# Kernel tuning notes

Hardware: AMD Instinct MI355X
Metric: run time of the kernel (lower is better)

The kernel has to match this reference:

```python
import jax, jax.numpy as jnp
import numpy as np

N = 100000      # nodes
E = 400000      # edges per relation
R = 4           # relations
DIN = 128       # input feat dim
DH = 128        # hidden_feat
NC = 16         # n_classes


def setup_inputs() -> dict:
    key = jax.random.key(0)
    ks = jax.random.split(key, 9)
    s = lambda d: 1.0 / np.sqrt(d)
    return {
        "x":  jax.random.normal(ks[0], (N, DIN), jnp.float32),
        "W0": jax.random.normal(ks[1], (R, DIN, DH), jnp.float32) * s(DIN),
        "b0": jnp.zeros((R, DH), jnp.float32),
        "W1": jax.random.normal(ks[2], (R, DH, DH), jnp.float32) * s(DH),
        "b1": jnp.zeros((R, DH), jnp.float32),
        "W2": jax.random.normal(ks[3], (R, DH, NC), jnp.float32) * s(DH),
        "b2": jnp.zeros((R, NC), jnp.float32),
        "src": jax.random.randint(ks[4], (R, E), 0, N, jnp.int32),
        "dst": jax.random.randint(ks[5], (R, E), 0, N, jnp.int32),
    }


def _graph_conv(h, W, b, s, d, act):
    """DGL GraphConv, norm='both': deg_out^-1/2 gather-matmul-scatter deg_in^-1/2."""
    ones = jnp.ones(s.shape[0], h.dtype)
    deg_out = jnp.clip(jax.ops.segment_sum(ones, s, num_segments=N), 1.0)  # [N]
    deg_in  = jnp.clip(jax.ops.segment_sum(ones, d, num_segments=N), 1.0)  # [N]
    hn = (h * jax.lax.rsqrt(deg_out)[:, None]) @ W           # [N, dout] (mm before aggregate)
    agg = jax.ops.segment_sum(hn[s], d, num_segments=N)      # scatter-sum over edges
    out = agg * jax.lax.rsqrt(deg_in)[:, None] + b
    return jax.nn.relu(out) if act else out


def _hetero_layer(h, W, b, src, dst, act):
    # HeteroGraphConv(aggregate='mean'): per-relation GraphConv then mean over relations
    outs = [_graph_conv(h, W[r], b[r], src[r], dst[r], act) for r in range(R)]
    return sum(outs) / R


def reference(x, W0, b0, W1, b1, W2, b2, src, dst):
    h = _hetero_layer(x, W0, b0, src, dst, act=True)
    h = _hetero_layer(h, W1, b1, src, dst, act=True)
    return _hetero_layer(h, W2, b2, src, dst, act=False)  # [N, NC] logits for target_node type
```

## Files before the change

kernel.cpp:

```cpp
#include <hip/hip_runtime.h>


#define NNODES 100000
#define NEDGE  400000
#define NREL   4
#define DHID   128
#define NCLS   16
#define SCANB  98

typedef _Float16 f16x8 __attribute__((ext_vector_type(8)));
typedef _Float16 f16x4 __attribute__((ext_vector_type(4)));
typedef float    f32x4 __attribute__((ext_vector_type(4)));

__global__ void edge_hist(const int* __restrict__ src, const int* __restrict__ dst,
                          int* __restrict__ cnt_out, int* __restrict__ cnt_in) {
    int e = blockIdx.x * 256 + threadIdx.x;
    int r = blockIdx.y;
    if (e < NEDGE) {
        atomicAdd(&cnt_out[r * NNODES + src[r * NEDGE + e]], 1);
        atomicAdd(&cnt_in [r * NNODES + dst[r * NEDGE + e]], 1);
    }
}

__global__ void rs_fin(const int* __restrict__ cnt_out, const int* __restrict__ cnt_in,
                       float* __restrict__ rs_out, float* __restrict__ rs_in) {
    int i = blockIdx.x * 256 + threadIdx.x;
    if (i < NREL * NNODES) {
        rs_out[i] = rsqrtf(fmaxf((float)cnt_out[i], 1.0f));
        rs_in [i] = rsqrtf(fmaxf((float)cnt_in [i], 1.0f));
    }
}

__global__ void scan1(const int* __restrict__ cnt, int* __restrict__ part) {
    __shared__ int sh[256];
    int r = blockIdx.y, b = blockIdx.x, tid = threadIdx.x;
    int n0 = b * 1024 + tid * 4;
    int s = 0;
#pragma unroll
    for (int j = 0; j < 4; ++j) {
        int n = n0 + j;
        s += (n < NNODES) ? cnt[r * NNODES + n] : 0;
    }
    sh[tid] = s; __syncthreads();
    for (int off = 128; off > 0; off >>= 1) {
        if (tid < off) sh[tid] += sh[tid + off];
        __syncthreads();
    }
    if (tid == 0) part[r * SCANB + b] = sh[0];
}

__global__ void scan2(int* __restrict__ part) {
    __shared__ int sh[128];
    int r = blockIdx.x, tid = threadIdx.x;
    int v = (tid < SCANB) ? part[r * SCANB + tid] : 0;
    sh[tid] = v; __syncthreads();
    for (int off = 1; off < 128; off <<= 1) {
        int t = (tid >= off) ? sh[tid - off] : 0;
        __syncthreads();
        sh[tid] += t;
        __syncthreads();
    }
    if (tid < SCANB) part[r * SCANB + tid] = sh[tid] - v;
}

__global__ void scan3(const int* __restrict__ cnt, const int* __restrict__ part,
                      int* __restrict__ ofs) {
    __shared__ int sh[256];
    int r = blockIdx.y, b = blockIdx.x, tid = threadIdx.x;
    int n0 = b * 1024 + tid * 4;
    int v[4];
    int tsum = 0;
#pragma unroll
    for (int j = 0; j < 4; ++j) {
        int n = n0 + j;
        v[j] = (n < NNODES) ? cnt[r * NNODES + n] : 0;
        tsum += v[j];
    }
    sh[tid] = tsum; __syncthreads();
    for (int off = 1; off < 256; off <<= 1) {
        int t = (tid >= off) ? sh[tid - off] : 0;
        __syncthreads();
        sh[tid] += t;
        __syncthreads();
    }
    int base = part[r * SCANB + b] + sh[tid] - tsum;
#pragma unroll
    for (int j = 0; j < 4; ++j) {
        int n = n0 + j;
        if (n < NNODES) ofs[r * (NNODES + 1) + n] = base;
        base += v[j];
    }
    if (b == 0 && tid == 0) ofs[r * (NNODES + 1) + NNODES] = NEDGE;
}

__global__ void csr_fill(const int* __restrict__ src, const int* __restrict__ dst,
                         const int* __restrict__ ofs, int* __restrict__ cnt_in,
                         const float* __restrict__ rs_out, int2* __restrict__ csrw) {
    int e = blockIdx.x * 256 + threadIdx.x;
    int r = blockIdx.y;
    if (e < NEDGE) {
        int s = src[r * NEDGE + e], d = dst[r * NEDGE + e];
        int k = atomicSub(&cnt_in[r * NNODES + d], 1) - 1;
        int2 ew;
        ew.x = s;
        ew.y = __float_as_int(rs_out[r * NNODES + s]);
        csrw[(size_t)r * NEDGE + ofs[r * (NNODES + 1) + d] + k] = ew;
    }
}

__global__ void wsplit(const float* __restrict__ W, _Float16* __restrict__ whi,
                       _Float16* __restrict__ wlo) {
    int idx = blockIdx.x * 256 + threadIdx.x;
    int c = idx & 127, k = (idx >> 7) & 127, r = idx >> 14;
    float w = W[(size_t)r * 16384 + k * 128 + c];
    _Float16 hi = (_Float16)w;
    size_t o = (((size_t)r * 16 + (k >> 3)) * 128 + c) * 8 + (k & 7);
    whi[o] = hi;
    wlo[o] = (_Float16)(w - (float)hi);
}

__global__ void wsplit2(const float* __restrict__ W2, _Float16* __restrict__ wh,
                        _Float16* __restrict__ wl) {
    int idx = blockIdx.x * 256 + threadIdx.x;
    if (idx < NREL * DHID * NCLS) {
        int c = idx & 15, k = (idx >> 4) & 127, r = idx >> 11;
        float w = W2[idx];
        _Float16 hi = (_Float16)w;
        size_t o = ((size_t)(k >> 3) * 64 + r * 16 + c) * 8 + (k & 7);
        wh[o] = hi;
        wl[o] = (_Float16)(w - (float)hi);
    }
}

__global__ void xcvt(const float* __restrict__ x, _Float16* __restrict__ xh) {
    int i = blockIdx.x * 256 + threadIdx.x;
    if (i < NNODES * DHID / 4) {
        float4 v = ((const float4*)x)[i];
        f16x4 h = {(_Float16)v.x, (_Float16)v.y, (_Float16)v.z, (_Float16)v.w};
        *(f16x4*)&xh[(size_t)i * 4] = h;
    }
}

__global__ __launch_bounds__(512) void gconv(
        const _Float16* __restrict__ Hh, const float* __restrict__ rs_in,
        const int* __restrict__ ofs, const int2* __restrict__ csrw,
        const _Float16* __restrict__ Wt_hi, const _Float16* __restrict__ Wt_lo,
        const float* __restrict__ bias, _Float16* __restrict__ outH) {
    __shared__ _Float16 lhi[4 * 16 * 67 * 8];
    __shared__ int lofs[NREL][65];
    int tid = threadIdx.x;
    int lane = tid & 63, wid = tid >> 6;
    int wm = wid >> 2, wn = wid & 3;
    int r15 = lane & 15;
    int row0 = blockIdx.x * 64;

    if (tid < 4 * 65) {
        int rel = tid / 65, i = tid - rel * 65;
        int n = row0 + i;
        lofs[rel][i] = (n <= NNODES) ? ofs[rel * (NNODES + 1) + n] : NEDGE;
    }
    __syncthreads();

    {
        int lane16 = tid & 15;
        int grp    = tid >> 4;
        const _Float16* hb = Hh + (size_t)lane16 * 8;
        for (int idx = grp; idx < 256; idx += 32) {
            int rel = idx >> 6, rr = idx & 63;
            int row = row0 + rr;
            float acc[8] = {};
            if (row < NNODES) {
                int i = lofs[rel][rr], end = lofs[rel][rr + 1];
                const int2* cw = csrw + (size_t)rel * NEDGE;
                for (; i + 4 <= end; i += 4) {
                    int2 e0 = cw[i], e1 = cw[i + 1], e2 = cw[i + 2], e3 = cw[i + 3];
                    f16x8 v0 = *(const f16x8*)(hb + (size_t)e0.x * DHID);
                    f16x8 v1 = *(const f16x8*)(hb + (size_t)e1.x * DHID);
                    f16x8 v2 = *(const f16x8*)(hb + (size_t)e2.x * DHID);
                    f16x8 v3 = *(const f16x8*)(hb + (size_t)e3.x * DHID);
                    float w0 = __int_as_float(e0.y), w1 = __int_as_float(e1.y);
                    float w2 = __int_as_float(e2.y), w3 = __int_as_float(e3.y);
#pragma unroll
                    for (int j = 0; j < 8; ++j)
                        acc[j] += ((float)v0[j] * w0 + (float)v1[j] * w1)
                                + ((float)v2[j] * w2 + (float)v3[j] * w3);
                }
                for (; i < end; ++i) {
                    int2 e = cw[i];
                    f16x8 v = *(const f16x8*)(hb + (size_t)e.x * DHID);
                    float w = __int_as_float(e.y);
#pragma unroll
                    for (int j = 0; j < 8; ++j) acc[j] += (float)v[j] * w;
                }
                float rv = rs_in[rel * NNODES + row];
#pragma unroll
                for (int j = 0; j < 8; ++j) acc[j] *= rv;
            }
            f16x8 o;
#pragma unroll
            for (int j = 0; j < 8; ++j) o[j] = (_Float16)acc[j];
            *(f16x8*)&lhi[(((rel * 16 + lane16) * 67) + rr) * 8] = o;
        }
    }
    __syncthreads();

    f32x4 oacc[2][2] = {};
    int kb = lane >> 4;
    int rbase = wm * 32 + r15;
    int c = wn * 32 + r15;
    for (int rel = 0; rel < NREL; ++rel) {
        f32x4 acc4[2][2] = {};
#pragma unroll
        for (int kt = 0; kt < 4; ++kt) {
            const _Float16* bh = Wt_hi + ((size_t)rel * 16 + kt * 4 + kb) * 128 * 8;
            const _Float16* bl = Wt_lo + ((size_t)rel * 16 + kt * 4 + kb) * 128 * 8;
            f16x8 wh[2], wl[2], ah[2];
#pragma unroll
            for (int nf = 0; nf < 2; ++nf) {
                wh[nf] = *(const f16x8*)(bh + (size_t)(c + nf * 16) * 8);
                wl[nf] = *(const f16x8*)(bl + (size_t)(c + nf * 16) * 8);
            }
#pragma unroll
            for (int mf = 0; mf < 2; ++mf) {
                int li = (((rel * 16 + kt * 4 + kb) * 67) + rbase + mf * 16) * 8;
                ah[mf] = *(const f16x8*)&lhi[li];
            }
#pragma unroll
            for (int nf = 0; nf < 2; ++nf)
#pragma unroll
                for (int mf = 0; mf < 2; ++mf) {
                    acc4[mf][nf] = __builtin_amdgcn_mfma_f32_16x16x32_f16(ah[mf], wh[nf], acc4[mf][nf], 0, 0, 0);
                    acc4[mf][nf] = __builtin_amdgcn_mfma_f32_16x16x32_f16(ah[mf], wl[nf], acc4[mf][nf], 0, 0, 0);
                }
        }
        const float* b = bias + rel * DHID;
#pragma unroll
        for (int mf = 0; mf < 2; ++mf)
#pragma unroll
            for (int nf = 0; nf < 2; ++nf) {
                float bb = b[wn * 32 + nf * 16 + r15];
#pragma unroll
                for (int i = 0; i < 4; ++i)
                    oacc[mf][nf][i] += fmaxf(acc4[mf][nf][i] + bb, 0.f);
            }
    }

    int rsub = (lane >> 4) * 4;
#pragma unroll
    for (int mf = 0; mf < 2; ++mf)
#pragma unroll
        for (int i = 0; i < 4; ++i) {
            int row = row0 + wm * 32 + mf * 16 + rsub + i;
            if (row < NNODES) {
#pragma unroll
                for (int nf = 0; nf < 2; ++nf) {
                    int cc = wn * 32 + nf * 16 + r15;
                    outH[(size_t)row * DHID + cc] = (_Float16)(oacc[mf][nf][i] * 0.25f);
                }
            }
        }
}

__global__ __launch_bounds__(256) void gemm64h(const _Float16* __restrict__ Hh,
                                               const _Float16* __restrict__ W2h,
                                               const _Float16* __restrict__ W2l,
                                               float* __restrict__ hw) {
    int tid = threadIdx.x, lane = tid & 63, wid = tid >> 6;
    int row0 = blockIdx.x * 64;
    int arow = row0 + wid * 16 + (lane & 15);
    int kb = lane >> 4;
    f32x4 acc[4] = {};
#pragma unroll
    for (int kt = 0; kt < 4; ++kt) {
        f16x8 a = {};
        if (arow < NNODES)
            a = *(const f16x8*)&Hh[(size_t)arow * DHID + kt * 32 + kb * 8];
        const _Float16* bh = W2h + ((size_t)(kt * 4 + kb) * 64) * 8;
        const _Float16* bl = W2l + ((size_t)(kt * 4 + kb) * 64) * 8;
#pragma unroll
        for (int nf = 0; nf < 4; ++nf) {
            f16x8 wh = *(const f16x8*)(bh + (size_t)(nf * 16 + (lane & 15)) * 8);
            f16x8 wl = *(const f16x8*)(bl + (size_t)(nf * 16 + (lane & 15)) * 8);
            acc[nf] = __builtin_amdgcn_mfma_f32_16x16x32_f16(a, wh, acc[nf], 0, 0, 0);
            acc[nf] = __builtin_amdgcn_mfma_f32_16x16x32_f16(a, wl, acc[nf], 0, 0, 0);
        }
    }
    int rsub = (lane >> 4) * 4;
#pragma unroll
    for (int nf = 0; nf < 4; ++nf)
#pragma unroll
        for (int i = 0; i < 4; ++i) {
            int row = row0 + wid * 16 + rsub + i;
            if (row < NNODES) hw[(size_t)row * 64 + nf * 16 + (lane & 15)] = acc[nf][i];
        }
}

__global__ __launch_bounds__(256) void l2_out(const float* __restrict__ hw,
                                              const int* __restrict__ ofs,
                                              const int2* __restrict__ csrw,
                                              const float* __restrict__ rs_in,
                                              const float* __restrict__ b2,
                                              float* __restrict__ out) {
    int t = threadIdx.x;
    int d = blockIdx.x * 4 + (t >> 6);
    int lane = t & 63;
    int r = lane >> 4;
    int c = lane & 15;
    if (d >= NNODES) return;
    int i   = ofs[r * (NNODES + 1) + d];
    int end = ofs[r * (NNODES + 1) + d + 1];
    const int2* cw = csrw + (size_t)r * NEDGE;
    float acc = 0.f;
    for (; i + 2 <= end; i += 2) {
        int2 e0 = cw[i], e1 = cw[i + 1];
        acc += hw[(size_t)e0.x * 64 + r * NCLS + c] * __int_as_float(e0.y)
             + hw[(size_t)e1.x * 64 + r * NCLS + c] * __int_as_float(e1.y);
    }
    for (; i < end; ++i) {
        int2 e = cw[i];
        acc += hw[(size_t)e.x * 64 + r * NCLS + c] * __int_as_float(e.y);
    }
    float tot = acc * rs_in[r * NNODES + d] + b2[r * NCLS + c];
    tot += __shfl_xor(tot, 16, 64);
    tot += __shfl_xor(tot, 32, 64);
    if (r == 0) out[(size_t)d * NCLS + c] = tot * 0.25f;
}

extern "C" void kernel_launch(void* const* d_in, const int* in_sizes, int n_in,
                              void* d_out, int out_size, void* d_ws, size_t ws_size,
                              hipStream_t stream) {
    const float* x  = (const float*)d_in[0];
    const float* W0 = (const float*)d_in[1];
    const float* b0 = (const float*)d_in[2];
    const float* W1 = (const float*)d_in[3];
    const float* b1 = (const float*)d_in[4];
    const float* W2 = (const float*)d_in[5];
    const float* b2 = (const float*)d_in[6];
    const int*   src = (const int*)d_in[7];
    const int*   dst = (const int*)d_in[8];
    float* out = (float*)d_out;

    char* p = (char*)d_ws;
    int2* csrw   = (int2*)p;           p += sizeof(int2) * (size_t)NREL * NEDGE;
    float* hw    = (float*)p;          p += sizeof(float) * (size_t)NNODES * 64;
    int* cnt_out = (int*)p;            p += sizeof(int) * NREL * NNODES;
    int* cnt_in  = (int*)p;            p += sizeof(int) * NREL * NNODES;
    int* ofs     = (int*)p;            p += sizeof(int) * NREL * (NNODES + 1) + 12;
    int* part    = (int*)p;            p += sizeof(int) * NREL * 128;
    float* rs_out = (float*)p;         p += sizeof(float) * NREL * NNODES;
    float* rs_in  = (float*)p;         p += sizeof(float) * NREL * NNODES;
    _Float16* Wt0h = (_Float16*)p;     p += sizeof(_Float16) * NREL * DHID * DHID;
    _Float16* Wt0l = (_Float16*)p;     p += sizeof(_Float16) * NREL * DHID * DHID;
    _Float16* Wt1h = (_Float16*)p;     p += sizeof(_Float16) * NREL * DHID * DHID;
    _Float16* Wt1l = (_Float16*)p;     p += sizeof(_Float16) * NREL * DHID * DHID;
    _Float16* W2h  = (_Float16*)p;     p += sizeof(_Float16) * 16 * 64 * 8;
    _Float16* W2l  = (_Float16*)p;     p += sizeof(_Float16) * 16 * 64 * 8;
    _Float16* xh   = (_Float16*)p;     p += sizeof(_Float16) * (size_t)NNODES * DHID;
    _Float16* h1   = (_Float16*)p;     p += sizeof(_Float16) * (size_t)NNODES * DHID;
    _Float16* h2   = (_Float16*)p;     p += sizeof(_Float16) * (size_t)NNODES * DHID;

    hipMemsetAsync(cnt_out, 0, 2ull * NREL * NNODES * sizeof(int), stream);
    dim3 eg((NEDGE + 255) / 256, NREL);
    edge_hist<<<eg, 256, 0, stream>>>(src, dst, cnt_out, cnt_in);
    rs_fin<<<(NREL * NNODES + 255) / 256, 256, 0, stream>>>(cnt_out, cnt_in, rs_out, rs_in);
    dim3 sg(SCANB, NREL);
    scan1<<<sg, 256, 0, stream>>>(cnt_in, part);
    scan2<<<NREL, 128, 0, stream>>>(part);
    scan3<<<sg, 256, 0, stream>>>(cnt_in, part, ofs);
    csr_fill<<<eg, 256, 0, stream>>>(src, dst, ofs, cnt_in, rs_out, csrw);

    wsplit<<<256, 256, 0, stream>>>(W0, Wt0h, Wt0l);
    wsplit<<<256, 256, 0, stream>>>(W1, Wt1h, Wt1l);
    wsplit2<<<32, 256, 0, stream>>>(W2, W2h, W2l);
    xcvt<<<(NNODES * DHID / 4 + 255) / 256, 256, 0, stream>>>(x, xh);

    int gb = (NNODES + 63) / 64;

    gconv<<<gb, 512, 0, stream>>>(xh, rs_in, ofs, csrw, Wt0h, Wt0l, b0, h1);
    gconv<<<gb, 512, 0, stream>>>(h1, rs_in, ofs, csrw, Wt1h, Wt1l, b1, h2);

    gemm64h<<<gb, 256, 0, stream>>>(h2, W2h, W2l, hw);
    l2_out<<<(NNODES + 3) / 4, 256, 0, stream>>>(hw, ofs, csrw, rs_in, b2, out);
}
```

Baseline: 686.9 us.

## Interleave four rows per thread in gather, store layer-2 projection in fp16

```diff
diff --git a/kernel.cpp b/kernel.cpp
--- a/kernel.cpp
+++ b/kernel.cpp
@@ -165,13 +165,47 @@
         int lane16 = tid & 15;
         int grp    = tid >> 4;
         const _Float16* hb = Hh + (size_t)lane16 * 8;
-        for (int idx = grp; idx < 256; idx += 32) {
-            int rel = idx >> 6, rr = idx & 63;
-            int row = row0 + rr;
-            float acc[8] = {};
-            if (row < NNODES) {
-                int i = lofs[rel][rr], end = lofs[rel][rr + 1];
-                const int2* cw = csrw + (size_t)rel * NEDGE;
+#pragma unroll
+        for (int s = 0; s < 2; ++s) {
+            int rel[4], rr[4], ii[4], ee[4];
+            float acc[4][8] = {};
+#pragma unroll
+            for (int k = 0; k < 4; ++k) {
+                int u = grp + s * 128 + k * 32;
+                rel[k] = u >> 6; rr[k] = u & 63;
+                ii[k] = lofs[rel[k]][rr[k]];
+                ee[k] = lofs[rel[k]][rr[k] + 1];
+                if (row0 + rr[k] >= NNODES) { ii[k] = 0; ee[k] = 0; }
+            }
+            while (ii[0] + 2 <= ee[0] && ii[1] + 2 <= ee[1] &&
+                   ii[2] + 2 <= ee[2] && ii[3] + 2 <= ee[3]) {
+                int2 ed[4][2];
+                f16x8 v[4][2];
+#pragma unroll
+                for (int k = 0; k < 4; ++k) {
+                    const int2* cw = csrw + (size_t)rel[k] * NEDGE;
+                    ed[k][0] = cw[ii[k]];
+                    ed[k][1] = cw[ii[k] + 1];
+                }
+#pragma unroll
+                for (int k = 0; k < 4; ++k) {
+                    v[k][0] = *(const f16x8*)(hb + (size_t)ed[k][0].x * DHID);
+                    v[k][1] = *(const f16x8*)(hb + (size_t)ed[k][1].x * DHID);
+                }
+#pragma unroll
+                for (int k = 0; k < 4; ++k) {
+                    float w0 = __int_as_float(ed[k][0].y);
+                    float w1 = __int_as_float(ed[k][1].y);
+#pragma unroll
+                    for (int j = 0; j < 8; ++j)
+                        acc[k][j] += (float)v[k][0][j] * w0 + (float)v[k][1][j] * w1;
+                    ii[k] += 2;
+                }
+            }
+#pragma unroll
+            for (int k = 0; k < 4; ++k) {
+                const int2* cw = csrw + (size_t)rel[k] * NEDGE;
+                int i = ii[k], end = ee[k];
                 for (; i + 4 <= end; i += 4) {
                     int2 e0 = cw[i], e1 = cw[i + 1], e2 = cw[i + 2], e3 = cw[i + 3];
                     f16x8 v0 = *(const f16x8*)(hb + (size_t)e0.x * DHID);
@@ -182,24 +216,23 @@
                     float w2 = __int_as_float(e2.y), w3 = __int_as_float(e3.y);
 #pragma unroll
                     for (int j = 0; j < 8; ++j)
-                        acc[j] += ((float)v0[j] * w0 + (float)v1[j] * w1)
-                                + ((float)v2[j] * w2 + (float)v3[j] * w3);
+                        acc[k][j] += ((float)v0[j] * w0 + (float)v1[j] * w1)
+                                   + ((float)v2[j] * w2 + (float)v3[j] * w3);
                 }
                 for (; i < end; ++i) {
                     int2 e = cw[i];
                     f16x8 v = *(const f16x8*)(hb + (size_t)e.x * DHID);
                     float w = __int_as_float(e.y);
 #pragma unroll
-                    for (int j = 0; j < 8; ++j) acc[j] += (float)v[j] * w;
-                }
-                float rv = rs_in[rel * NNODES + row];
-#pragma unroll
-                for (int j = 0; j < 8; ++j) acc[j] *= rv;
-            }
-            f16x8 o;
-#pragma unroll
-            for (int j = 0; j < 8; ++j) o[j] = (_Float16)acc[j];
-            *(f16x8*)&lhi[(((rel * 16 + lane16) * 67) + rr) * 8] = o;
+                    for (int j = 0; j < 8; ++j) acc[k][j] += (float)v[j] * w;
+                }
+                int row = row0 + rr[k];
+                float rv = (row < NNODES) ? rs_in[rel[k] * NNODES + row] : 0.f;
+                f16x8 o;
+#pragma unroll
+                for (int j = 0; j < 8; ++j) o[j] = (_Float16)(acc[k][j] * rv);
+                *(f16x8*)&lhi[(((rel[k] * 16 + lane16) * 67) + rr[k]) * 8] = o;
+            }
         }
     }
     __syncthreads();
@@ -264,7 +297,7 @@
 __global__ __launch_bounds__(256) void gemm64h(const _Float16* __restrict__ Hh,
                                                const _Float16* __restrict__ W2h,
                                                const _Float16* __restrict__ W2l,
-                                               float* __restrict__ hw) {
+                                               _Float16* __restrict__ hw) {
     int tid = threadIdx.x, lane = tid & 63, wid = tid >> 6;
     int row0 = blockIdx.x * 64;
     int arow = row0 + wid * 16 + (lane & 15);
@@ -291,11 +324,12 @@
 #pragma unroll
         for (int i = 0; i < 4; ++i) {
             int row = row0 + wid * 16 + rsub + i;
-            if (row < NNODES) hw[(size_t)row * 64 + nf * 16 + (lane & 15)] = acc[nf][i];
+            if (row < NNODES)
+                hw[(size_t)row * 64 + nf * 16 + (lane & 15)] = (_Float16)acc[nf][i];
         }
 }
 
-__global__ __launch_bounds__(256) void l2_out(const float* __restrict__ hw,
+__global__ __launch_bounds__(256) void l2_out(const _Float16* __restrict__ hw,
                                               const int* __restrict__ ofs,
                                               const int2* __restrict__ csrw,
                                               const float* __restrict__ rs_in,
@@ -311,14 +345,18 @@
     int end = ofs[r * (NNODES + 1) + d + 1];
     const int2* cw = csrw + (size_t)r * NEDGE;
     float acc = 0.f;
-    for (; i + 2 <= end; i += 2) {
-        int2 e0 = cw[i], e1 = cw[i + 1];
-        acc += hw[(size_t)e0.x * 64 + r * NCLS + c] * __int_as_float(e0.y)
-             + hw[(size_t)e1.x * 64 + r * NCLS + c] * __int_as_float(e1.y);
+    for (; i + 4 <= end; i += 4) {
+        int2 e0 = cw[i], e1 = cw[i + 1], e2 = cw[i + 2], e3 = cw[i + 3];
+        float v0 = (float)hw[(size_t)e0.x * 64 + r * NCLS + c];
+        float v1 = (float)hw[(size_t)e1.x * 64 + r * NCLS + c];
+        float v2 = (float)hw[(size_t)e2.x * 64 + r * NCLS + c];
+        float v3 = (float)hw[(size_t)e3.x * 64 + r * NCLS + c];
+        acc += v0 * __int_as_float(e0.y) + v1 * __int_as_float(e1.y)
+             + v2 * __int_as_float(e2.y) + v3 * __int_as_float(e3.y);
     }
     for (; i < end; ++i) {
         int2 e = cw[i];
-        acc += hw[(size_t)e.x * 64 + r * NCLS + c] * __int_as_float(e.y);
+        acc += (float)hw[(size_t)e.x * 64 + r * NCLS + c] * __int_as_float(e.y);
     }
     float tot = acc * rs_in[r * NNODES + d] + b2[r * NCLS + c];
     tot += __shfl_xor(tot, 16, 64);
@@ -342,7 +380,6 @@
 
     char* p = (char*)d_ws;
     int2* csrw   = (int2*)p;           p += sizeof(int2) * (size_t)NREL * NEDGE;
-    float* hw    = (float*)p;          p += sizeof(float) * (size_t)NNODES * 64;
     int* cnt_out = (int*)p;            p += sizeof(int) * NREL * NNODES;
     int* cnt_in  = (int*)p;            p += sizeof(int) * NREL * NNODES;
     int* ofs     = (int*)p;            p += sizeof(int) * NREL * (NNODES + 1) + 12;
@@ -358,6 +395,7 @@
     _Float16* xh   = (_Float16*)p;     p += sizeof(_Float16) * (size_t)NNODES * DHID;
     _Float16* h1   = (_Float16*)p;     p += sizeof(_Float16) * (size_t)NNODES * DHID;
     _Float16* h2   = (_Float16*)p;     p += sizeof(_Float16) * (size_t)NNODES * DHID;
+    _Float16* hw   = (_Float16*)p;     p += sizeof(_Float16) * (size_t)NNODES * 64;
 
     hipMemsetAsync(cnt_out, 0, 2ull * NREL * NNODES * sizeof(int), stream);
     dim3 eg((NEDGE + 255) / 256, NREL);
```

After: 686.8 us. No clear change (-0.0%).
